# Kernel tuning notes

Measured on AMD Instinct MI355X. Metric: run time of the kernel, lower is better.

The kernel has to match this reference:

```python
import jax, jax.numpy as jnp
import numpy as np

D, DEPTH, H, DH, K, BINS = 192, 12, 6, 32, 32, 65


def _ln(x, s, b):
    mu = jnp.mean(x, -1, keepdims=True)
    var = jnp.mean((x - mu) ** 2, -1, keepdims=True)
    return (x - mu) / jnp.sqrt(var + 1e-5) * s + b


def setup_inputs() -> dict:
    key = jax.random.key(0)
    ks = jax.random.split(key, 24)
    B, L = 32, 512
    w = lambda k, shp: jax.random.normal(k, shp, jnp.float32) * 0.02
    return {
        "seq": jax.random.randint(ks[0], (B, L), 0, 4, jnp.int32),
        "mask": jnp.ones((B, L), jnp.bool_),
        "bppm": jax.random.uniform(ks[1], (B, L, L), jnp.float32),
        "emb": w(ks[2], (4, D)),
        "pair_w": w(ks[3], (H, 1)), "pair_b": jnp.zeros((H,), jnp.float32),
        "relpos_w": w(ks[4], (H, BINS)), "relpos_b": jnp.zeros((H,), jnp.float32),
        "ln1_s": jnp.ones((DEPTH, D), jnp.float32), "ln1_b": jnp.zeros((DEPTH, D), jnp.float32),
        "qkv_w": w(ks[5], (DEPTH, 3 * D, D)), "qkv_b": jnp.zeros((DEPTH, 3 * D), jnp.float32),
        "out_w": w(ks[6], (DEPTH, D, D)), "out_b": jnp.zeros((DEPTH, D), jnp.float32),
        "ln2_s": jnp.ones((DEPTH, D), jnp.float32), "ln2_b": jnp.zeros((DEPTH, D), jnp.float32),
        "ff1_w": w(ks[7], (DEPTH, 4 * D, D)), "ff1_b": jnp.zeros((DEPTH, 4 * D), jnp.float32),
        "ff2_w": w(ks[8], (DEPTH, D, 4 * D)), "ff2_b": jnp.zeros((DEPTH, D), jnp.float32),
        "proj_w": w(ks[9], (2, D)), "proj_b": jnp.zeros((2,), jnp.float32),
    }


def reference(seq, mask, bppm, emb, pair_w, pair_b, relpos_w, relpos_b,
              ln1_s, ln1_b, qkv_w, qkv_b, out_w, out_b, ln2_s, ln2_b,
              ff1_w, ff1_b, ff2_w, ff2_b, proj_w, proj_b):
    B, L = seq.shape
    x = emb[seq]  # [B,L,D]
    # pairwise bias: linear_pair(bppm[...,None]) + linear_relpos(one_hot(rp))
    pair = bppm[..., None] * pair_w[:, 0] + pair_b  # [B,L,L,H]
    res = jnp.arange(L)
    rp = jnp.clip(res[:, None] - res[None, :], -K, K) + K  # [L,L]
    pos_enc = relpos_w.T[rp] + relpos_b  # one-hot @ W.T == gather rows of W.T
    bias = jnp.transpose(pair + pos_enc[None], (0, 3, 1, 2))  # [B,H,L,L]
    keep = mask[:, None, None, :]  # key padding over keys
    scale = 1.0 / jnp.sqrt(jnp.float32(DH))
    for i in range(DEPTH):
        h = _ln(x, ln1_s[i], ln1_b[i])
        qkv = h @ qkv_w[i].T + qkv_b[i]  # [B,L,3D]
        q, k, v = jnp.split(qkv, 3, axis=-1)
        q = q.reshape(B, L, H, DH); k = k.reshape(B, L, H, DH); v = v.reshape(B, L, H, DH)
        scores = jnp.einsum("bqhd,bkhd->bhqk", q, k) * scale + bias
        scores = jnp.where(keep, scores, -1e9)
        attn = jax.nn.softmax(scores, axis=-1)
        o = jnp.einsum("bhqk,bkhd->bqhd", attn, v).reshape(B, L, D)
        x = x + (o @ out_w[i].T + out_b[i])
        h = _ln(x, ln2_s[i], ln2_b[i])
        ff = jax.nn.gelu(h @ ff1_w[i].T + ff1_b[i], approximate=False)
        x = x + (ff @ ff2_w[i].T + ff2_b[i])
    return x @ proj_w.T + proj_b  # [B,L,2]
```

## Files before the change

### kernel.cpp

```cpp
#include <hip/hip_runtime.h>
#include <hip/hip_bf16.h>

#define B_    32
#define L_    512
#define D_    192
#define DEPTH_ 12
#define H_    6
#define DH_   32
#define NR    (B_*L_)

typedef unsigned short u16;
typedef __attribute__((ext_vector_type(8))) short short8;
typedef __attribute__((ext_vector_type(4))) float f32x4;

__device__ __forceinline__ float b2f(u16 u){ union{unsigned int i; float f;} v; v.i=((unsigned)u)<<16; return v.f; }
__device__ __forceinline__ u16 f2b(float f){ __hip_bfloat16 h = __float2bfloat16(f); return *reinterpret_cast<u16*>(&h); }
__device__ __forceinline__ float b2f_lo(unsigned dw){ union{unsigned int i; float f;} v; v.i=dw<<16; return v.f; }
__device__ __forceinline__ float b2f_hi(unsigned dw){ union{unsigned int i; float f;} v; v.i=dw&0xffff0000u; return v.f; }

__device__ __forceinline__ void gll16(const u16* g, u16* l){
    __builtin_amdgcn_global_load_lds((const __attribute__((address_space(1))) unsigned int*)g,
                                     (__attribute__((address_space(3))) unsigned int*)l, 16, 0, 0);
}

__global__ __launch_bounds__(256) void k_cvt(const float* __restrict__ src, u16* __restrict__ dst, int n4){
    int i = blockIdx.x*256 + threadIdx.x;
    if (i >= n4) return;
    float4 v = reinterpret_cast<const float4*>(src)[i];
    ushort4 o; o.x=f2b(v.x); o.y=f2b(v.y); o.z=f2b(v.z); o.w=f2b(v.w);
    reinterpret_cast<ushort4*>(dst)[i] = o;
}

__global__ __launch_bounds__(256) void k_bprep(const float* __restrict__ bppm, u16* __restrict__ bp){
    int tid = threadIdx.x; int w = tid>>6, lane = tid&63, quad = lane>>4, l16 = lane&15;
    int blk = blockIdx.x; int b = blk>>6, qt = (blk>>3)&7, kt = blk&7;
    const float* src = bppm + (size_t)(b*L_ + qt*64 + w*16 + quad*4)*L_ + kt*64 + l16;
    u16 vals[16];
    #pragma unroll
    for(int ni=0;ni<4;ni++)
        #pragma unroll
        for(int r=0;r<4;r++)
            vals[ni*4+r] = f2b(src[(size_t)r*L_ + ni*16]);
    u16* dst = bp + ((size_t)((((b*8+qt)*4+w)*8+kt)*64 + lane))*16;
    *reinterpret_cast<uint4*>(dst)   = *reinterpret_cast<uint4*>(vals);
    *reinterpret_cast<uint4*>(dst+8) = *reinterpret_cast<uint4*>(vals+8);
}

__global__ void k_embed(const int* __restrict__ seq, const float* __restrict__ emb, float* __restrict__ x){
    int i = blockIdx.x*blockDim.x + threadIdx.x;
    if (i >= NR*D_) return;
    int row = i / D_; int d = i - row*D_;
    x[i] = emb[seq[row]*D_ + d];
}

__global__ __launch_bounds__(256) void k_ln(const float* __restrict__ x, const float* __restrict__ s,
                                            const float* __restrict__ b, u16* __restrict__ h){
    int row  = blockIdx.x*4 + (threadIdx.x>>6);
    int lane = threadIdx.x & 63;
    const float* xr = x + (size_t)row*D_;
    float v0=xr[lane], v1=xr[lane+64], v2=xr[lane+128];
    float sum = v0+v1+v2;
    #pragma unroll
    for(int off=32; off; off>>=1) sum += __shfl_xor(sum, off);
    float mu = sum * (1.f/192.f);
    float d0=v0-mu, d1=v1-mu, d2=v2-mu;
    float vs = d0*d0+d1*d1+d2*d2;
    #pragma unroll
    for(int off=32; off; off>>=1) vs += __shfl_xor(vs, off);
    float rstd = rsqrtf(vs*(1.f/192.f) + 1e-5f);
    u16* hr = h + (size_t)row*D_;
    hr[lane]     = f2b(d0*rstd*s[lane]     + b[lane]);
    hr[lane+64]  = f2b(d1*rstd*s[lane+64]  + b[lane+64]);
    hr[lane+128] = f2b(d2*rstd*s[lane+128] + b[lane+128]);
}

template<int EPI>
__global__ __launch_bounds__(256) void k_gemm(const u16* __restrict__ A, const u16* __restrict__ W,
                                              const float* __restrict__ bias,
                                              u16* __restrict__ out, float* __restrict__ xres,
                                              u16* __restrict__ vt,
                                              int M, int N, int K){
    __shared__ __align__(16) u16 As[128*64];
    __shared__ __align__(16) u16 Ws[64*64];
    int tid = threadIdx.x;
    int n0 = blockIdx.x*64, m0 = blockIdx.y*128;
    int w = tid>>6, lane = tid&63, quad = lane>>4, l16 = lane&15;
    int wm = w>>1, wn = w&1;
    int wbase = tid & ~63;
    f32x4 zero = {0.f,0.f,0.f,0.f};
    f32x4 acc[4][2];
    #pragma unroll
    for(int a=0;a<4;a++){ acc[a][0]=zero; acc[a][1]=zero; }
    int nchunks = K>>6;
    for(int kc=0; kc<nchunks; kc++){
        int kbase = kc<<6;
        #pragma unroll
        for(int i=0;i<4;i++){
            int L = tid + (i<<8);
            int r = L>>3;
            int gseg = (L&7) ^ (r&7);
            gll16(&A[(size_t)(m0+r)*K + kbase + gseg*8], &As[(size_t)(wbase + (i<<8))*8]);
        }
        #pragma unroll
        for(int i=0;i<2;i++){
            int L = tid + (i<<8);
            int r = L>>3;
            int gseg = (L&7) ^ (r&7);
            gll16(&W[(size_t)(n0+r)*K + kbase + gseg*8], &Ws[(size_t)(wbase + (i<<8))*8]);
        }
        __syncthreads();
        #pragma unroll
        for(int kk=0; kk<64; kk+=32){
            int sw = ((kk>>3) + quad) ^ (l16&7);
            short8 af[4], bf[2];
            #pragma unroll
            for(int mi=0;mi<4;mi++) af[mi] = *reinterpret_cast<const short8*>(&As[(wm*64+mi*16+l16)*64 + sw*8]);
            #pragma unroll
            for(int ni=0;ni<2;ni++) bf[ni] = *reinterpret_cast<const short8*>(&Ws[(wn*32+ni*16+l16)*64 + sw*8]);
            #pragma unroll
            for(int mi=0;mi<4;mi++)
                #pragma unroll
                for(int ni=0;ni<2;ni++)
                    acc[mi][ni] = __builtin_amdgcn_mfma_f32_16x16x32_bf16(af[mi], bf[ni], acc[mi][ni], 0,0,0);
        }
        __syncthreads();
    }
    #pragma unroll
    for(int mi=0;mi<4;mi++){
        int row = m0 + wm*64 + mi*16 + quad*4;
        #pragma unroll
        for(int ni=0;ni<2;ni++){
            int col = n0 + wn*32 + ni*16 + l16;
            float bv = bias[col];
            float v[4];
            #pragma unroll
            for(int r=0;r<4;r++) v[r] = acc[mi][ni][r] + bv;
            if (EPI==1){
                #pragma unroll
                for(int r=0;r<4;r++){
                    float g = 0.5f*v[r]*(1.f + erff(v[r]*0.70710678f));
                    out[(size_t)(row+r)*N + col] = f2b(g);
                }
            } else if (EPI==2){
                #pragma unroll
                for(int r=0;r<4;r++) xres[(size_t)(row+r)*D_ + col] += v[r];
            } else {
                if (col < 384){
                    #pragma unroll
                    for(int r=0;r<4;r++) out[(size_t)(row+r)*N + col] = f2b(v[r]);
                } else {
                    int hh = (col-384)>>5, dh = (col-384)&31;
                    int bq = row>>9, l = row&511;
                    ushort4 t; t.x=f2b(v[0]); t.y=f2b(v[1]); t.z=f2b(v[2]); t.w=f2b(v[3]);
                    *reinterpret_cast<ushort4*>(&vt[((size_t)(bq*H_+hh)*32 + dh)*512 + l]) = t;
                }
            }
        }
    }
}

__global__ __launch_bounds__(256) void k_attn(const u16* __restrict__ qkv, const u16* __restrict__ vt,
                                              const u16* __restrict__ bp,
                                              const float* __restrict__ pair_w, const float* __restrict__ pair_b,
                                              const float* __restrict__ relw, const float* __restrict__ relb,
                                              u16* __restrict__ o){
    __shared__ u16 Ps[4][16*88];
    __shared__ float relE[4][68];
    int tid = threadIdx.x;
    int blk = blockIdx.x;
    int b = blk/(H_*8); int rem = blk - b*(H_*8); int h = rem>>3; int qt = rem&7;
    int q0 = qt*64;
    int w = tid>>6, lane = tid&63, quad = lane>>4, l16 = lane&15;
    const float LOG2E = 1.4426950408889634f;
    float pwE  = pair_w[h]*LOG2E;
    float addE = (pair_b[h] + relb[h])*LOG2E;
    relE[w][lane] = relw[h*65 + (lane>64?64:lane)]*LOG2E + addE;
    if (lane==0) relE[w][64] = relw[h*65 + 64]*LOG2E + addE;
    const float scaleE = 0.17677669529663687f*LOG2E;
    short8 qf = *reinterpret_cast<const short8*>(&qkv[(size_t)(b*L_ + q0 + w*16 + l16)*576 + h*32 + quad*8]);
    const u16* kbase = qkv + (size_t)b*L_*576 + 192 + h*32 + quad*8 + (size_t)l16*576;
    const u16* vbase = vt + ((size_t)(b*H_+h)*32 + l16)*512 + quad*8;
    const u16* bbase = bp + (size_t)(((b*8+qt)*4+w)*8)*1024 + (size_t)lane*16;
    f32x4 zero = {0.f,0.f,0.f,0.f};
    f32x4 accO0 = zero, accO1 = zero;
    float l_acc[4] = {0.f,0.f,0.f,0.f};
    short8 kf0 = *reinterpret_cast<const short8*>(&kbase[0]);
    short8 kf1 = *reinterpret_cast<const short8*>(&kbase[16*576]);
    short8 kf2 = *reinterpret_cast<const short8*>(&kbase[32*576]);
    short8 kf3 = *reinterpret_cast<const short8*>(&kbase[48*576]);
    uint4 bt0 = *reinterpret_cast<const uint4*>(&bbase[0]);
    uint4 bt1 = *reinterpret_cast<const uint4*>(&bbase[8]);
    for(int kt=0; kt<8; kt++){
        int kn = (kt+1)&7;
        size_t kon = (size_t)kn*64*576;
        short8 nk0 = *reinterpret_cast<const short8*>(&kbase[kon]);
        short8 nk1 = *reinterpret_cast<const short8*>(&kbase[kon+16*576]);
        short8 nk2 = *reinterpret_cast<const short8*>(&kbase[kon+32*576]);
        short8 nk3 = *reinterpret_cast<const short8*>(&kbase[kon+48*576]);
        uint4 nb0 = *reinterpret_cast<const uint4*>(&bbase[(size_t)kn*1024]);
        uint4 nb1 = *reinterpret_cast<const uint4*>(&bbase[(size_t)kn*1024+8]);
        short8 vf00 = *reinterpret_cast<const short8*>(&vbase[(size_t)kt*64]);
        short8 vf01 = *reinterpret_cast<const short8*>(&vbase[(size_t)kt*64 + 16*512]);
        short8 vf10 = *reinterpret_cast<const short8*>(&vbase[(size_t)kt*64 + 32]);
        short8 vf11 = *reinterpret_cast<const short8*>(&vbase[(size_t)kt*64 + 16*512 + 32]);
        f32x4 sv[4];
        sv[0] = __builtin_amdgcn_mfma_f32_16x16x32_bf16(qf, kf0, zero, 0,0,0);
        sv[1] = __builtin_amdgcn_mfma_f32_16x16x32_bf16(qf, kf1, zero, 0,0,0);
        sv[2] = __builtin_amdgcn_mfma_f32_16x16x32_bf16(qf, kf2, zero, 0,0,0);
        sv[3] = __builtin_amdgcn_mfma_f32_16x16x32_bf16(qf, kf3, zero, 0,0,0);
        unsigned bw[8] = {bt0.x,bt0.y,bt0.z,bt0.w,bt1.x,bt1.y,bt1.z,bt1.w};
        bool far = (qt-kt>=2) | (kt-qt>=2);
        float relc = relE[w][qt>kt ? 64 : 0];
        int k0 = kt*64;
        #pragma unroll
        for(int ni=0; ni<2; ni++){
            #pragma unroll
            for(int r=0; r<4; r++){
                int j = ni*4+r;
                float bb = (j&1) ? b2f_hi(bw[j>>1]) : b2f_lo(bw[j>>1]);
                float relv;
                if (far) relv = relc;
                else {
                    int dlt = (q0 + w*16 + quad*4 + r) - (k0 + ni*16 + l16);
                    dlt = dlt < -32 ? -32 : (dlt > 32 ? 32 : dlt);
                    relv = relE[w][dlt + 32];
                }
                float pe = exp2f(fmaf(sv[ni][r], scaleE, fmaf(bb, pwE, relv)));
                u16 pr = f2b(pe);
                Ps[w][(quad*4+r)*88 + ni*16 + l16] = pr;
                l_acc[r] += b2f(pr);
            }
        }
        short8 pf0 = *reinterpret_cast<const short8*>(&Ps[w][l16*88 + quad*8]);
        accO0 = __builtin_amdgcn_mfma_f32_16x16x32_bf16(pf0, vf00, accO0, 0,0,0);
        accO1 = __builtin_amdgcn_mfma_f32_16x16x32_bf16(pf0, vf01, accO1, 0,0,0);
        #pragma unroll
        for(int ni=2; ni<4; ni++){
            #pragma unroll
            for(int r=0; r<4; r++){
                int j = ni*4+r;
                float bb = (j&1) ? b2f_hi(bw[j>>1]) : b2f_lo(bw[j>>1]);
                float relv;
                if (far) relv = relc;
                else {
                    int dlt = (q0 + w*16 + quad*4 + r) - (k0 + ni*16 + l16);
                    dlt = dlt < -32 ? -32 : (dlt > 32 ? 32 : dlt);
                    relv = relE[w][dlt + 32];
                }
                float pe = exp2f(fmaf(sv[ni][r], scaleE, fmaf(bb, pwE, relv)));
                u16 pr = f2b(pe);
                Ps[w][(quad*4+r)*88 + ni*16 + l16] = pr;
                l_acc[r] += b2f(pr);
            }
        }
        short8 pf1 = *reinterpret_cast<const short8*>(&Ps[w][l16*88 + 32 + quad*8]);
        accO0 = __builtin_amdgcn_mfma_f32_16x16x32_bf16(pf1, vf10, accO0, 0,0,0);
        accO1 = __builtin_amdgcn_mfma_f32_16x16x32_bf16(pf1, vf11, accO1, 0,0,0);
        kf0=nk0; kf1=nk1; kf2=nk2; kf3=nk3; bt0=nb0; bt1=nb1;
    }
    #pragma unroll
    for(int r=0;r<4;r++){
        #pragma unroll
        for(int off=1; off<16; off<<=1) l_acc[r] += __shfl_xor(l_acc[r], off);
    }
    #pragma unroll
    for(int r=0;r<4;r++){
        int qg = q0 + w*16 + quad*4 + r;
        float inv = 1.f / l_acc[r];
        o[(size_t)(b*L_ + qg)*D_ + h*32 + l16]      = f2b(accO0[r] * inv);
        o[(size_t)(b*L_ + qg)*D_ + h*32 + 16 + l16] = f2b(accO1[r] * inv);
    }
}

__global__ __launch_bounds__(256) void k_proj(const float* __restrict__ x, const float* __restrict__ pw,
                                              const float* __restrict__ pb, float* __restrict__ out){
    int row  = blockIdx.x*4 + (threadIdx.x>>6);
    int lane = threadIdx.x & 63;
    const float* xr = x + (size_t)row*D_;
    float s0=0.f, s1=0.f;
    #pragma unroll
    for(int j=0;j<3;j++){
        float xv = xr[lane + 64*j];
        s0 += xv * pw[lane + 64*j];
        s1 += xv * pw[192 + lane + 64*j];
    }
    #pragma unroll
    for(int off=32; off; off>>=1){ s0 += __shfl_xor(s0, off); s1 += __shfl_xor(s1, off); }
    if (lane==0){
        out[(size_t)row*2 + 0] = s0 + pb[0];
        out[(size_t)row*2 + 1] = s1 + pb[1];
    }
}

extern "C" void kernel_launch(void* const* d_in, const int* in_sizes, int n_in,
                              void* d_out, int out_size, void* d_ws, size_t ws_size,
                              hipStream_t stream){
    const int*   seq    = (const int*)d_in[0];
    const float* bppm   = (const float*)d_in[2];
    const float* emb    = (const float*)d_in[3];
    const float* pair_w = (const float*)d_in[4];
    const float* pair_b = (const float*)d_in[5];
    const float* relw   = (const float*)d_in[6];
    const float* relb   = (const float*)d_in[7];
    const float* ln1s   = (const float*)d_in[8];
    const float* ln1b   = (const float*)d_in[9];
    const float* qkvw   = (const float*)d_in[10];
    const float* qkvb   = (const float*)d_in[11];
    const float* outw   = (const float*)d_in[12];
    const float* outb   = (const float*)d_in[13];
    const float* ln2s   = (const float*)d_in[14];
    const float* ln2b   = (const float*)d_in[15];
    const float* ff1w   = (const float*)d_in[16];
    const float* ff1b   = (const float*)d_in[17];
    const float* ff2w   = (const float*)d_in[18];
    const float* ff2b   = (const float*)d_in[19];
    const float* projw  = (const float*)d_in[20];
    const float* projb  = (const float*)d_in[21];

    char* ws = (char*)d_ws;
    float* x   = (float*)ws;  ws += (size_t)NR*D_*4;
    u16*  h    = (u16*)ws;    ws += (size_t)NR*D_*2;
    u16*  qkv  = (u16*)ws;    ws += (size_t)NR*576*2;
    u16*  o    = (u16*)ws;    ws += (size_t)NR*D_*2;
    u16*  ff   = (u16*)ws;    ws += (size_t)NR*768*2;
    u16* qkvw_h = (u16*)ws;   ws += (size_t)DEPTH_*576*D_*2;
    u16* outw_h = (u16*)ws;   ws += (size_t)DEPTH_*D_*D_*2;
    u16* ff1w_h = (u16*)ws;   ws += (size_t)DEPTH_*768*D_*2;
    u16* ff2w_h = (u16*)ws;   ws += (size_t)DEPTH_*D_*768*2;
    u16* bp     = (u16*)ws;   ws += (size_t)B_*L_*L_*2;
    u16* vt     = (u16*)ws;   ws += (size_t)B_*H_*DH_*L_*2;

    {
        int n;
        n = DEPTH_*576*D_/4; k_cvt<<<(n+255)/256, 256, 0, stream>>>(qkvw, qkvw_h, n);
        n = DEPTH_*D_*D_/4;  k_cvt<<<(n+255)/256, 256, 0, stream>>>(outw, outw_h, n);
        n = DEPTH_*768*D_/4; k_cvt<<<(n+255)/256, 256, 0, stream>>>(ff1w, ff1w_h, n);
        n = DEPTH_*D_*768/4; k_cvt<<<(n+255)/256, 256, 0, stream>>>(ff2w, ff2w_h, n);
        k_bprep<<<B_*8*8, 256, 0, stream>>>(bppm, bp);
    }

    k_embed<<<(NR*D_+255)/256, 256, 0, stream>>>(seq, emb, x);
    for(int i=0;i<DEPTH_;i++){
        k_ln<<<NR/4, 256, 0, stream>>>(x, ln1s+i*D_, ln1b+i*D_, h);
        k_gemm<3><<<dim3(576/64, NR/128), 256, 0, stream>>>(h, qkvw_h+(size_t)i*576*D_, qkvb+i*576, qkv, nullptr, vt, NR, 576, D_);
        k_attn<<<B_*H_*8, 256, 0, stream>>>(qkv, vt, bp, pair_w, pair_b, relw, relb, o);
        k_gemm<2><<<dim3(192/64, NR/128), 256, 0, stream>>>(o, outw_h+(size_t)i*D_*D_, outb+i*D_, nullptr, x, nullptr, NR, D_, D_);
        k_ln<<<NR/4, 256, 0, stream>>>(x, ln2s+i*D_, ln2b+i*D_, h);
        k_gemm<1><<<dim3(768/64, NR/128), 256, 0, stream>>>(h, ff1w_h+(size_t)i*768*D_, ff1b+i*768, ff, nullptr, nullptr, NR, 768, D_);
        k_gemm<2><<<dim3(192/64, NR/128), 256, 0, stream>>>(ff, ff2w_h+(size_t)i*D_*768, ff2b+i*D_, nullptr, x, nullptr, NR, D_, 768);
    }
    k_proj<<<NR/4, 256, 0, stream>>>(x, projw, projb, (float*)d_out);
}
```

Before: 1.652 ms.

## Switch bf16 to fp16 and split attention keys across eight waves

All intermediate storage and MFMA ops move from bf16 to fp16. The attention kernel now runs 512 threads per block: two query groups of 32 rows and four key groups, each wave covering two key tiles. Partial outputs and row sums are reduced through LDS at the end. This gives more waves per block and more parallelism per query tile, at the cost of an extra LDS reduction and fp16 range risk, since exp is taken without max subtraction and fp16 overflows above 65504.

```diff
diff --git a/kernel.cpp b/kernel.cpp
--- a/kernel.cpp
+++ b/kernel.cpp
@@ -1,5 +1,5 @@
 #include <hip/hip_runtime.h>
-#include <hip/hip_bf16.h>
+#include <hip/hip_fp16.h>
 
 #define B_    32
 #define L_    512
@@ -10,13 +10,13 @@
 #define NR    (B_*L_)
 
 typedef unsigned short u16;
-typedef __attribute__((ext_vector_type(8))) short short8;
+typedef __attribute__((ext_vector_type(8))) _Float16 half8;
 typedef __attribute__((ext_vector_type(4))) float f32x4;
 
-__device__ __forceinline__ float b2f(u16 u){ union{unsigned int i; float f;} v; v.i=((unsigned)u)<<16; return v.f; }
-__device__ __forceinline__ u16 f2b(float f){ __hip_bfloat16 h = __float2bfloat16(f); return *reinterpret_cast<u16*>(&h); }
-__device__ __forceinline__ float b2f_lo(unsigned dw){ union{unsigned int i; float f;} v; v.i=dw<<16; return v.f; }
-__device__ __forceinline__ float b2f_hi(unsigned dw){ union{unsigned int i; float f;} v; v.i=dw&0xffff0000u; return v.f; }
+__device__ __forceinline__ float h2f(u16 u){ __half h = *reinterpret_cast<__half*>(&u); return __half2float(h); }
+__device__ __forceinline__ u16 f2h(float f){ __half h = __float2half(f); return *reinterpret_cast<u16*>(&h); }
+__device__ __forceinline__ float h2f_lo(unsigned dw){ return h2f((u16)(dw & 0xffffu)); }
+__device__ __forceinline__ float h2f_hi(unsigned dw){ return h2f((u16)(dw >> 16)); }
 
 __device__ __forceinline__ void gll16(const u16* g, u16* l){
     __builtin_amdgcn_global_load_lds((const __attribute__((address_space(1))) unsigned int*)g,
@@ -27,7 +27,7 @@
     int i = blockIdx.x*256 + threadIdx.x;
     if (i >= n4) return;
     float4 v = reinterpret_cast<const float4*>(src)[i];
-    ushort4 o; o.x=f2b(v.x); o.y=f2b(v.y); o.z=f2b(v.z); o.w=f2b(v.w);
+    ushort4 o; o.x=f2h(v.x); o.y=f2h(v.y); o.z=f2h(v.z); o.w=f2h(v.w);
     reinterpret_cast<ushort4*>(dst)[i] = o;
 }
 
@@ -40,7 +40,7 @@
     for(int ni=0;ni<4;ni++)
         #pragma unroll
         for(int r=0;r<4;r++)
-            vals[ni*4+r] = f2b(src[(size_t)r*L_ + ni*16]);
+            vals[ni*4+r] = f2h(src[(size_t)r*L_ + ni*16]);
     u16* dst = bp + ((size_t)((((b*8+qt)*4+w)*8+kt)*64 + lane))*16;
     *reinterpret_cast<uint4*>(dst)   = *reinterpret_cast<uint4*>(vals);
     *reinterpret_cast<uint4*>(dst+8) = *reinterpret_cast<uint4*>(vals+8);
@@ -69,9 +69,9 @@
     for(int off=32; off; off>>=1) vs += __shfl_xor(vs, off);
     float rstd = rsqrtf(vs*(1.f/192.f) + 1e-5f);
     u16* hr = h + (size_t)row*D_;
-    hr[lane]     = f2b(d0*rstd*s[lane]     + b[lane]);
-    hr[lane+64]  = f2b(d1*rstd*s[lane+64]  + b[lane+64]);
-    hr[lane+128] = f2b(d2*rstd*s[lane+128] + b[lane+128]);
+    hr[lane]     = f2h(d0*rstd*s[lane]     + b[lane]);
+    hr[lane+64]  = f2h(d1*rstd*s[lane+64]  + b[lane+64]);
+    hr[lane+128] = f2h(d2*rstd*s[lane+128] + b[lane+128]);
 }
 
 template<int EPI>
@@ -112,16 +112,16 @@
         #pragma unroll
         for(int kk=0; kk<64; kk+=32){
             int sw = ((kk>>3) + quad) ^ (l16&7);
-            short8 af[4], bf[2];
-            #pragma unroll
-            for(int mi=0;mi<4;mi++) af[mi] = *reinterpret_cast<const short8*>(&As[(wm*64+mi*16+l16)*64 + sw*8]);
-            #pragma unroll
-            for(int ni=0;ni<2;ni++) bf[ni] = *reinterpret_cast<const short8*>(&Ws[(wn*32+ni*16+l16)*64 + sw*8]);
+            half8 af[4], bf[2];
+            #pragma unroll
+            for(int mi=0;mi<4;mi++) af[mi] = *reinterpret_cast<const half8*>(&As[(wm*64+mi*16+l16)*64 + sw*8]);
+            #pragma unroll
+            for(int ni=0;ni<2;ni++) bf[ni] = *reinterpret_cast<const half8*>(&Ws[(wn*32+ni*16+l16)*64 + sw*8]);
             #pragma unroll
             for(int mi=0;mi<4;mi++)
                 #pragma unroll
                 for(int ni=0;ni<2;ni++)
-                    acc[mi][ni] = __builtin_amdgcn_mfma_f32_16x16x32_bf16(af[mi], bf[ni], acc[mi][ni], 0,0,0);
+                    acc[mi][ni] = __builtin_amdgcn_mfma_f32_16x16x32_f16(af[mi], bf[ni], acc[mi][ni], 0,0,0);
         }
         __syncthreads();
     }
@@ -139,7 +139,7 @@
                 #pragma unroll
                 for(int r=0;r<4;r++){
                     float g = 0.5f*v[r]*(1.f + erff(v[r]*0.70710678f));
-                    out[(size_t)(row+r)*N + col] = f2b(g);
+                    out[(size_t)(row+r)*N + col] = f2h(g);
                 }
             } else if (EPI==2){
                 #pragma unroll
@@ -147,11 +147,11 @@
             } else {
                 if (col < 384){
                     #pragma unroll
-                    for(int r=0;r<4;r++) out[(size_t)(row+r)*N + col] = f2b(v[r]);
+                    for(int r=0;r<4;r++) out[(size_t)(row+r)*N + col] = f2h(v[r]);
                 } else {
                     int hh = (col-384)>>5, dh = (col-384)&31;
                     int bq = row>>9, l = row&511;
-                    ushort4 t; t.x=f2b(v[0]); t.y=f2b(v[1]); t.z=f2b(v[2]); t.w=f2b(v[3]);
+                    ushort4 t; t.x=f2h(v[0]); t.y=f2h(v[1]); t.z=f2h(v[2]); t.w=f2h(v[3]);
                     *reinterpret_cast<ushort4*>(&vt[((size_t)(bq*H_+hh)*32 + dh)*512 + l]) = t;
                 }
             }
@@ -159,116 +159,125 @@
     }
 }
 
-__global__ __launch_bounds__(256) void k_attn(const u16* __restrict__ qkv, const u16* __restrict__ vt,
+__global__ __launch_bounds__(512) void k_attn(const u16* __restrict__ qkv, const u16* __restrict__ vt,
                                               const u16* __restrict__ bp,
                                               const float* __restrict__ pair_w, const float* __restrict__ pair_b,
                                               const float* __restrict__ relw, const float* __restrict__ relb,
                                               u16* __restrict__ o){
-    __shared__ u16 Ps[4][16*88];
-    __shared__ float relE[4][68];
+    __shared__ __align__(16) float redbuf[8*64*25];
+    __shared__ float relE[8][68];
+    u16* Ps = (u16*)redbuf;
+    float* red = redbuf;
     int tid = threadIdx.x;
     int blk = blockIdx.x;
     int b = blk/(H_*8); int rem = blk - b*(H_*8); int h = rem>>3; int qt = rem&7;
     int q0 = qt*64;
     int w = tid>>6, lane = tid&63, quad = lane>>4, l16 = lane&15;
+    int qg = w>>2, kg = w&3;
     const float LOG2E = 1.4426950408889634f;
     float pwE  = pair_w[h]*LOG2E;
     float addE = (pair_b[h] + relb[h])*LOG2E;
-    relE[w][lane] = relw[h*65 + (lane>64?64:lane)]*LOG2E + addE;
+    relE[w][lane] = relw[h*65 + lane]*LOG2E + addE;
     if (lane==0) relE[w][64] = relw[h*65 + 64]*LOG2E + addE;
     const float scaleE = 0.17677669529663687f*LOG2E;
-    short8 qf = *reinterpret_cast<const short8*>(&qkv[(size_t)(b*L_ + q0 + w*16 + l16)*576 + h*32 + quad*8]);
-    const u16* kbase = qkv + (size_t)b*L_*576 + 192 + h*32 + quad*8 + (size_t)l16*576;
-    const u16* vbase = vt + ((size_t)(b*H_+h)*32 + l16)*512 + quad*8;
-    const u16* bbase = bp + (size_t)(((b*8+qt)*4+w)*8)*1024 + (size_t)lane*16;
+    half8 qf[2];
+    #pragma unroll
+    for(int mi=0;mi<2;mi++)
+        qf[mi] = *reinterpret_cast<const half8*>(&qkv[(size_t)(b*L_ + q0 + qg*32 + mi*16 + l16)*576 + h*32 + quad*8]);
     f32x4 zero = {0.f,0.f,0.f,0.f};
-    f32x4 accO0 = zero, accO1 = zero;
-    float l_acc[4] = {0.f,0.f,0.f,0.f};
-    short8 kf0 = *reinterpret_cast<const short8*>(&kbase[0]);
-    short8 kf1 = *reinterpret_cast<const short8*>(&kbase[16*576]);
-    short8 kf2 = *reinterpret_cast<const short8*>(&kbase[32*576]);
-    short8 kf3 = *reinterpret_cast<const short8*>(&kbase[48*576]);
-    uint4 bt0 = *reinterpret_cast<const uint4*>(&bbase[0]);
-    uint4 bt1 = *reinterpret_cast<const uint4*>(&bbase[8]);
-    for(int kt=0; kt<8; kt++){
-        int kn = (kt+1)&7;
-        size_t kon = (size_t)kn*64*576;
-        short8 nk0 = *reinterpret_cast<const short8*>(&kbase[kon]);
-        short8 nk1 = *reinterpret_cast<const short8*>(&kbase[kon+16*576]);
-        short8 nk2 = *reinterpret_cast<const short8*>(&kbase[kon+32*576]);
-        short8 nk3 = *reinterpret_cast<const short8*>(&kbase[kon+48*576]);
-        uint4 nb0 = *reinterpret_cast<const uint4*>(&bbase[(size_t)kn*1024]);
-        uint4 nb1 = *reinterpret_cast<const uint4*>(&bbase[(size_t)kn*1024+8]);
-        short8 vf00 = *reinterpret_cast<const short8*>(&vbase[(size_t)kt*64]);
-        short8 vf01 = *reinterpret_cast<const short8*>(&vbase[(size_t)kt*64 + 16*512]);
-        short8 vf10 = *reinterpret_cast<const short8*>(&vbase[(size_t)kt*64 + 32]);
-        short8 vf11 = *reinterpret_cast<const short8*>(&vbase[(size_t)kt*64 + 16*512 + 32]);
-        f32x4 sv[4];
-        sv[0] = __builtin_amdgcn_mfma_f32_16x16x32_bf16(qf, kf0, zero, 0,0,0);
-        sv[1] = __builtin_amdgcn_mfma_f32_16x16x32_bf16(qf, kf1, zero, 0,0,0);
-        sv[2] = __builtin_amdgcn_mfma_f32_16x16x32_bf16(qf, kf2, zero, 0,0,0);
-        sv[3] = __builtin_amdgcn_mfma_f32_16x16x32_bf16(qf, kf3, zero, 0,0,0);
-        unsigned bw[8] = {bt0.x,bt0.y,bt0.z,bt0.w,bt1.x,bt1.y,bt1.z,bt1.w};
-        bool far = (qt-kt>=2) | (kt-qt>=2);
-        float relc = relE[w][qt>kt ? 64 : 0];
+    f32x4 accO[2][2]; accO[0][0]=zero; accO[0][1]=zero; accO[1][0]=zero; accO[1][1]=zero;
+    float l_acc[2][4] = {{0.f,0.f,0.f,0.f},{0.f,0.f,0.f,0.f}};
+    u16* PsW = Ps + w*2304;
+    #pragma unroll
+    for(int j=0;j<2;j++){
+        int kt = kg + j*4;
         int k0 = kt*64;
-        #pragma unroll
-        for(int ni=0; ni<2; ni++){
-            #pragma unroll
-            for(int r=0; r<4; r++){
-                int j = ni*4+r;
-                float bb = (j&1) ? b2f_hi(bw[j>>1]) : b2f_lo(bw[j>>1]);
-                float relv;
-                if (far) relv = relc;
-                else {
-                    int dlt = (q0 + w*16 + quad*4 + r) - (k0 + ni*16 + l16);
-                    dlt = dlt < -32 ? -32 : (dlt > 32 ? 32 : dlt);
-                    relv = relE[w][dlt + 32];
+        half8 kf[4];
+        #pragma unroll
+        for(int ni=0;ni<4;ni++)
+            kf[ni] = *reinterpret_cast<const half8*>(&qkv[(size_t)(b*L_ + k0 + ni*16 + l16)*576 + 192 + h*32 + quad*8]);
+        half8 vf[2][2];
+        #pragma unroll
+        for(int t=0;t<2;t++)
+            #pragma unroll
+            for(int kki=0;kki<2;kki++)
+                vf[t][kki] = *reinterpret_cast<const half8*>(&vt[((size_t)(b*H_+h)*32 + t*16 + l16)*512 + k0 + kki*32 + quad*8]);
+        bool far = (qt-kt>=2)|(kt-qt>=2);
+        float relc = relE[w][qt>kt?64:0];
+        #pragma unroll
+        for(int mi=0;mi<2;mi++){
+            const u16* bb_p = &bp[((size_t)(((b*8+qt)*4 + qg*2+mi)*8 + kt)*64 + lane)*16];
+            uint4 bt0 = *reinterpret_cast<const uint4*>(bb_p);
+            uint4 bt1 = *reinterpret_cast<const uint4*>(bb_p+8);
+            unsigned bw[8] = {bt0.x,bt0.y,bt0.z,bt0.w,bt1.x,bt1.y,bt1.z,bt1.w};
+            f32x4 sv[4];
+            #pragma unroll
+            for(int ni=0;ni<4;ni++)
+                sv[ni] = __builtin_amdgcn_mfma_f32_16x16x32_f16(qf[mi], kf[ni], zero, 0,0,0);
+            #pragma unroll
+            for(int ni=0;ni<4;ni++){
+                #pragma unroll
+                for(int r=0;r<4;r++){
+                    int jj = ni*4+r;
+                    float bb = (jj&1)? h2f_hi(bw[jj>>1]) : h2f_lo(bw[jj>>1]);
+                    float relv;
+                    if (far) relv = relc;
+                    else {
+                        int dlt = (q0 + qg*32 + mi*16 + quad*4 + r) - (k0 + ni*16 + l16);
+                        dlt = dlt < -32 ? -32 : (dlt > 32 ? 32 : dlt);
+                        relv = relE[w][dlt+32];
+                    }
+                    float pe = exp2f(fmaf(sv[ni][r], scaleE, fmaf(bb, pwE, relv)));
+                    u16 pr = f2h(pe);
+                    PsW[(mi*16 + quad*4 + r)*72 + ni*16 + l16] = pr;
+                    l_acc[mi][r] += h2f(pr);
                 }
-                float pe = exp2f(fmaf(sv[ni][r], scaleE, fmaf(bb, pwE, relv)));
-                u16 pr = f2b(pe);
-                Ps[w][(quad*4+r)*88 + ni*16 + l16] = pr;
-                l_acc[r] += b2f(pr);
             }
         }
-        short8 pf0 = *reinterpret_cast<const short8*>(&Ps[w][l16*88 + quad*8]);
-        accO0 = __builtin_amdgcn_mfma_f32_16x16x32_bf16(pf0, vf00, accO0, 0,0,0);
-        accO1 = __builtin_amdgcn_mfma_f32_16x16x32_bf16(pf0, vf01, accO1, 0,0,0);
-        #pragma unroll
-        for(int ni=2; ni<4; ni++){
-            #pragma unroll
-            for(int r=0; r<4; r++){
-                int j = ni*4+r;
-                float bb = (j&1) ? b2f_hi(bw[j>>1]) : b2f_lo(bw[j>>1]);
-                float relv;
-                if (far) relv = relc;
-                else {
-                    int dlt = (q0 + w*16 + quad*4 + r) - (k0 + ni*16 + l16);
-                    dlt = dlt < -32 ? -32 : (dlt > 32 ? 32 : dlt);
-                    relv = relE[w][dlt + 32];
-                }
-                float pe = exp2f(fmaf(sv[ni][r], scaleE, fmaf(bb, pwE, relv)));
-                u16 pr = f2b(pe);
-                Ps[w][(quad*4+r)*88 + ni*16 + l16] = pr;
-                l_acc[r] += b2f(pr);
+        #pragma unroll
+        for(int kki=0;kki<2;kki++){
+            #pragma unroll
+            for(int mi=0;mi<2;mi++){
+                half8 pf = *reinterpret_cast<const half8*>(&PsW[(mi*16 + l16)*72 + kki*32 + quad*8]);
+                accO[mi][0] = __builtin_amdgcn_mfma_f32_16x16x32_f16(pf, vf[0][kki], accO[mi][0], 0,0,0);
+                accO[mi][1] = __builtin_amdgcn_mfma_f32_16x16x32_f16(pf, vf[1][kki], accO[mi][1], 0,0,0);
             }
         }
-        short8 pf1 = *reinterpret_cast<const short8*>(&Ps[w][l16*88 + 32 + quad*8]);
-        accO0 = __builtin_amdgcn_mfma_f32_16x16x32_bf16(pf1, vf10, accO0, 0,0,0);
-        accO1 = __builtin_amdgcn_mfma_f32_16x16x32_bf16(pf1, vf11, accO1, 0,0,0);
-        kf0=nk0; kf1=nk1; kf2=nk2; kf3=nk3; bt0=nb0; bt1=nb1;
+    }
+    #pragma unroll
+    for(int mi=0;mi<2;mi++)
+        #pragma unroll
+        for(int r=0;r<4;r++)
+            #pragma unroll
+            for(int off=1; off<16; off<<=1)
+                l_acc[mi][r] += __shfl_xor(l_acc[mi][r], off);
+    __syncthreads();
+    float* my = &red[(w*64 + lane)*25];
+    #pragma unroll
+    for(int mi=0;mi<2;mi++)
+        #pragma unroll
+        for(int t=0;t<2;t++)
+            #pragma unroll
+            for(int r=0;r<4;r++)
+                my[(mi*2+t)*4+r] = accO[mi][t][r];
+    #pragma unroll
+    for(int mi=0;mi<2;mi++)
+        #pragma unroll
+        for(int r=0;r<4;r++)
+            my[16+mi*4+r] = l_acc[mi][r];
+    __syncthreads();
+    int cmi = kg>>1, ct = kg&1;
+    float ov[4] = {0.f,0.f,0.f,0.f}, lv[4] = {0.f,0.f,0.f,0.f};
+    #pragma unroll
+    for(int kg2=0;kg2<4;kg2++){
+        const float* p = &red[((qg*4+kg2)*64 + lane)*25];
+        #pragma unroll
+        for(int r=0;r<4;r++){ ov[r] += p[(cmi*2+ct)*4+r]; lv[r] += p[16+cmi*4+r]; }
     }
     #pragma unroll
     for(int r=0;r<4;r++){
-        #pragma unroll
-        for(int off=1; off<16; off<<=1) l_acc[r] += __shfl_xor(l_acc[r], off);
-    }
-    #pragma unroll
-    for(int r=0;r<4;r++){
-        int qg = q0 + w*16 + quad*4 + r;
-        float inv = 1.f / l_acc[r];
-        o[(size_t)(b*L_ + qg)*D_ + h*32 + l16]      = f2b(accO0[r] * inv);
-        o[(size_t)(b*L_ + qg)*D_ + h*32 + 16 + l16] = f2b(accO1[r] * inv);
+        int qrow = q0 + qg*32 + cmi*16 + quad*4 + r;
+        o[(size_t)(b*L_ + qrow)*D_ + h*32 + ct*16 + l16] = f2h(ov[r]/lv[r]);
     }
 }
 
@@ -343,7 +352,7 @@
     for(int i=0;i<DEPTH_;i++){
         k_ln<<<NR/4, 256, 0, stream>>>(x, ln1s+i*D_, ln1b+i*D_, h);
         k_gemm<3><<<dim3(576/64, NR/128), 256, 0, stream>>>(h, qkvw_h+(size_t)i*576*D_, qkvb+i*576, qkv, nullptr, vt, NR, 576, D_);
-        k_attn<<<B_*H_*8, 256, 0, stream>>>(qkv, vt, bp, pair_w, pair_b, relw, relb, o);
+        k_attn<<<B_*H_*8, 512, 0, stream>>>(qkv, vt, bp, pair_w, pair_b, relw, relb, o);
         k_gemm<2><<<dim3(192/64, NR/128), 256, 0, stream>>>(o, outw_h+(size_t)i*D_*D_, outb+i*D_, nullptr, x, nullptr, NR, D_, D_);
         k_ln<<<NR/4, 256, 0, stream>>>(x, ln2s+i*D_, ln2b+i*D_, h);
         k_gemm<1><<<dim3(768/64, NR/128), 256, 0, stream>>>(h, ff1w_h+(size_t)i*768*D_, ff1b+i*768, ff, nullptr, nullptr, NR, 768, D_);
```

Measured after the change: 1.757 ms. 6.4% more time.
